# Performance work log

Hardware: AMD Instinct MI355X
Metric: run time of the kernel (lower is better)

The kernel has to match this reference:

```python
import jax, jax.numpy as jnp
import numpy as np

RATIO = 0.2
MIX_ALPHA = 0.5
TEMPERATURE = 0.1
EPS = 1e-12  # F.normalize eps


def setup_inputs() -> dict:
    key = jax.random.key(0)
    z = jax.random.normal(key, (16384, 256), dtype=jnp.float32)
    return {"z": z}


def reference(z):
    B = z.shape[0]
    n_hard = max(1, int(B * RATIO))

    # L2-normalize rows (F.normalize with eps clamp)
    norm = jnp.maximum(jnp.linalg.norm(z, axis=-1, keepdims=True), EPS)
    z_norm = z / norm

    # [B, B] cosine similarity, diagonal excluded
    sim = z_norm @ z_norm.T
    diag = jnp.eye(B, dtype=bool)
    sim = jnp.where(diag, -jnp.inf, sim)
    logits = sim / TEMPERATURE  # softmax(logits) == sim_probs

    # Batched sampling: replaces the per-sample Python loop with one fused pass
    key = jax.random.key(42)
    k_src, k_tgt, k_alpha = jax.random.split(key, 3)
    src_idx = jax.random.randint(k_src, (n_hard,), 0, B)  # torch.randint
    # categorical over logits rows == multinomial over softmax probs
    tgt_idx = jax.random.categorical(k_tgt, logits[src_idx], axis=-1)
    alpha = jax.random.uniform(k_alpha, (n_hard, 1), dtype=z.dtype) * MIX_ALPHA

    hard_negs = alpha * z[src_idx] + (1.0 - alpha) * z[tgt_idx]  # [n_hard, D]
    return hard_negs
```

## Files before the change

kernel.cpp:

```cpp
#include <hip/hip_runtime.h>
#include <stdint.h>
#include <math.h>

#define BN 16384
#define DK 256
#define NH 3276
#define NJB 52
#define NCB 128
#define NTILE (NJB * NCB)

typedef __attribute__((ext_vector_type(8))) short short8;
typedef __attribute__((ext_vector_type(4))) short short4v;
typedef __attribute__((ext_vector_type(4))) float f32x4;

__host__ __device__ __forceinline__ void tf2x32(uint32_t k0, uint32_t k1,
                                                uint32_t c0, uint32_t c1,
                                                uint32_t& o0, uint32_t& o1) {
  uint32_t ks2 = 0x1BD11BDAu ^ k0 ^ k1;
  uint32_t x0 = c0 + k0, x1 = c1 + k1;
#define RR(d) { x0 += x1; x1 = (x1 << d) | (x1 >> (32 - d)); x1 ^= x0; }
  RR(13) RR(15) RR(26) RR(6)   x0 += k1;  x1 += ks2 + 1u;
  RR(17) RR(29) RR(16) RR(24)  x0 += ks2; x1 += k0  + 2u;
  RR(13) RR(15) RR(26) RR(6)   x0 += k0;  x1 += k1  + 3u;
  RR(17) RR(29) RR(16) RR(24)  x0 += k1;  x1 += ks2 + 4u;
  RR(13) RR(15) RR(26) RR(6)   x0 += ks2; x1 += k0  + 5u;
#undef RR
  o0 = x0; o1 = x1;
}

__device__ __forceinline__ uint32_t rand32_at(uint32_t k0, uint32_t k1, uint32_t p) {
  uint32_t x0, x1; tf2x32(k0, k1, 0u, p, x0, x1);
  return x0 ^ x1;
}

__device__ __forceinline__ float unif01_from_bits(uint32_t bits) {
  return __uint_as_float((bits >> 9) | 0x3f800000u) - 1.0f;
}

__device__ __forceinline__ float gumbel_at(uint32_t k0, uint32_t k1, uint32_t p) {
  uint32_t bits = rand32_at(k0, k1, p);
  float f = unif01_from_bits(bits);
  float u = fmaxf(f, 1.17549435e-38f);
  float t = __log2f(u) * (-0.69314718055994531f);
  return __log2f(t) * (-0.69314718055994531f);
}

__device__ __forceinline__ unsigned long long packvc(float v, uint32_t c) {
  uint32_t u = __float_as_uint(v);
  u ^= ((int32_t)u < 0) ? 0xFFFFFFFFu : 0x80000000u;
  return ((unsigned long long)u << 32) | (unsigned long long)(~c);
}

__device__ __forceinline__ void glds16(const unsigned short* g, short* l) {
  __builtin_amdgcn_global_load_lds(
      (const __attribute__((address_space(1))) void*)g,
      (__attribute__((address_space(3))) void*)l, 16, 0, 0);
}

__global__ __launch_bounds__(256) void k_prep(const float* __restrict__ z,
                                              unsigned short* __restrict__ zh,
                                              unsigned short* __restrict__ zl,
                                              int* __restrict__ src_idx,
                                              unsigned long long* __restrict__ best,
                                              uint32_t k20, uint32_t k21) {
  int b = blockIdx.x, t = threadIdx.x;
  if (b < BN / 4) {
    int row = b * 4 + (t >> 6), lane = t & 63;
    float4 v = *(const float4*)&z[row * DK + lane * 4];
    float ss = v.x * v.x + v.y * v.y + v.z * v.z + v.w * v.w;
#pragma unroll
    for (int off = 32; off; off >>= 1) ss += __shfl_xor(ss, off, 64);
    float inv = 1.0f / fmaxf(sqrtf(ss), 1e-12f);
    float f[4] = {v.x * inv, v.y * inv, v.z * inv, v.w * inv};
    short4v h, l;
#pragma unroll
    for (int i = 0; i < 4; ++i) {
      uint32_t u = __float_as_uint(f[i]);
      h[i] = (short)(u >> 16);
      float r = f[i] - __uint_as_float(u & 0xFFFF0000u);
      l[i] = (short)(__float_as_uint(r) >> 16);
    }
    *(short4v*)&zh[row * DK + lane * 4] = h;
    *(short4v*)&zl[row * DK + lane * 4] = l;
  } else {
    int i = (b - BN / 4) * 256 + t;
    if (i < NH) {
      uint32_t bits = rand32_at(k20, k21, (uint32_t)i);
      src_idx[i] = (int)(bits & (uint32_t)(BN - 1));
      best[i] = 0ull;
    }
  }
}

__global__ __launch_bounds__(256, 4) void k_main(const unsigned short* __restrict__ zh,
                                                 const unsigned short* __restrict__ zl,
                                                 const int* __restrict__ src_idx,
                                                 unsigned long long* __restrict__ best,
                                                 uint32_t kt0, uint32_t kt1) {
  __shared__ __align__(16) short As_hi[64 * 32];
  __shared__ __align__(16) short As_lo[64 * 32];
  __shared__ __align__(16) short Bs_hi[128 * 32];
  __shared__ __align__(16) short Bs_lo[128 * 32];

  const int flat = blockIdx.x;
  const int xcd = flat & 7, slot = flat >> 3;
  const int c_base = (xcd * 16 + (slot & 15)) * 128;
  const int j_base = (slot >> 4) * 64;

  const int t = threadIdx.x;
  const int lane = t & 63, w = t >> 6;

  const int ra = w * 16 + (lane >> 2);
  const int rb0 = w * 32 + (lane >> 2);
  const int rb1 = rb0 + 16;
  const int ua = (lane & 3) ^ ((ra >> 1) & 3);
  const int ub0 = (lane & 3) ^ ((rb0 >> 1) & 3);
  const int ub1 = (lane & 3) ^ ((rb1 >> 1) & 3);
  const uint32_t offA = (uint32_t)(src_idx[min(j_base + ra, NH - 1)] * DK + ua * 8);
  const uint32_t offB0 = (uint32_t)((c_base + rb0) * DK + ub0 * 8);
  const uint32_t offB1 = (uint32_t)((c_base + rb1) * DK + ub1 * 8);
  short* dA  = &As_hi[w * 512];
  short* dAl = &As_lo[w * 512];
  short* dB  = &Bs_hi[w * 1024];
  short* dBl = &Bs_lo[w * 1024];

  const int mh = w >> 1, ch = w & 1;
  const int cl = lane & 15, q = lane >> 4;
  int foffA[2], foffB[4];
#pragma unroll
  for (int i = 0; i < 2; ++i) {
    int r = mh * 32 + cl + i * 16;
    foffA[i] = r * 32 + (q ^ ((r >> 1) & 3)) * 8;
  }
#pragma unroll
  for (int i = 0; i < 4; ++i) {
    int r = ch * 64 + cl + i * 16;
    foffB[i] = r * 32 + (q ^ ((r >> 1) & 3)) * 8;
  }

  const int q4 = q * 4;
  const int coff = c_base + ch * 64;
  const int roff = j_base + mh * 32;
  const uint32_t ccl = (uint32_t)(coff + cl);

  f32x4 acc[2][4];
#pragma unroll
  for (int mt = 0; mt < 2; ++mt)
#pragma unroll
    for (int nt = 0; nt < 4; ++nt) acc[mt][nt] = (f32x4){0.f, 0.f, 0.f, 0.f};

  float gum[32];

  glds16(zh + offA, dA);
  glds16(zl + offA, dAl);
  glds16(zh + offB0, dB);
  glds16(zh + offB1, dB + 512);
  glds16(zl + offB0, dBl);
  glds16(zl + offB1, dBl + 512);

#pragma unroll
  for (int kc = 0; kc < 8; ++kc) {
    __syncthreads();

    short8 ah[2], al[2], bh[4], bl[4];
#pragma unroll
    for (int nt = 0; nt < 4; ++nt) {
      bh[nt] = *(const short8*)&Bs_hi[foffB[nt]];
      bl[nt] = *(const short8*)&Bs_lo[foffB[nt]];
    }
#pragma unroll
    for (int mt = 0; mt < 2; ++mt) {
      ah[mt] = *(const short8*)&As_hi[foffA[mt]];
      al[mt] = *(const short8*)&As_lo[foffA[mt]];
    }
    __syncthreads();

    if (kc < 7) {
      const int ko = (kc + 1) * 32;
      glds16(zh + offA + ko, dA);
      glds16(zl + offA + ko, dAl);
      glds16(zh + offB0 + ko, dB);
      glds16(zh + offB1 + ko, dB + 512);
      glds16(zl + offB0 + ko, dBl);
      glds16(zl + offB1 + ko, dBl + 512);
    }

#pragma unroll
    for (int mt = 0; mt < 2; ++mt)
#pragma unroll
      for (int nt = 0; nt < 4; ++nt) {
        acc[mt][nt] = __builtin_amdgcn_mfma_f32_16x16x32_bf16(ah[mt], bh[nt], acc[mt][nt], 0, 0, 0);
        acc[mt][nt] = __builtin_amdgcn_mfma_f32_16x16x32_bf16(ah[mt], bl[nt], acc[mt][nt], 0, 0, 0);
        acc[mt][nt] = __builtin_amdgcn_mfma_f32_16x16x32_bf16(al[mt], bh[nt], acc[mt][nt], 0, 0, 0);
      }

#pragma unroll
    for (int i = 0; i < 4; ++i) {
      const int idx = kc * 4 + i;
      const int mt = idx >> 4, r = (idx >> 2) & 3, nt = idx & 3;
      int gj = roff + mt * 16 + q4 + r;
      uint32_t p = (uint32_t)gj * (uint32_t)BN + ccl + (uint32_t)(nt * 16);
      float gv = gumbel_at(kt0, kt1, p);
      asm volatile("" : "+v"(gv));
      gum[idx] = gv;
    }
  }

#pragma unroll
  for (int mt = 0; mt < 2; ++mt)
#pragma unroll
    for (int r = 0; r < 4; ++r) {
      int gj = roff + mt * 16 + q4 + r;
      int s = src_idx[min(gj, NH - 1)];
      float bv = -INFINITY; uint32_t bc = 0;
#pragma unroll
      for (int nt = 0; nt < 4; ++nt) {
        uint32_t c = ccl + (uint32_t)(nt * 16);
        float tot = fmaf(acc[mt][nt][r], 10.0f, gum[((mt * 4 + r) * 4) + nt]);
        tot = ((int)c == s) ? -INFINITY : tot;
        if (tot > bv) { bv = tot; bc = c; }
      }
      unsigned long long key = packvc(bv, bc);
#pragma unroll
      for (int off = 1; off <= 8; off <<= 1) {
        unsigned long long o = __shfl_xor(key, off, 64);
        if (o > key) key = o;
      }
      if (cl == 0 && gj < NH) atomicMax(&best[gj], key);
    }
}

__global__ __launch_bounds__(64) void k_out(const float* __restrict__ z,
                                            const int* __restrict__ src_idx,
                                            const unsigned long long* __restrict__ best,
                                            float* __restrict__ out,
                                            uint32_t ka0, uint32_t ka1) {
  int j = blockIdx.x;
  int lane = threadIdx.x;
  int s = src_idx[j];
  int tgt = (int)(~((uint32_t)(best[j] & 0xFFFFFFFFull)));
  uint32_t bits = rand32_at(ka0, ka1, (uint32_t)j);
  float alpha = unif01_from_bits(bits) * 0.5f;
  float om = 1.0f - alpha;
  float4 a = *(const float4*)&z[s * DK + lane * 4];
  float4 b = *(const float4*)&z[tgt * DK + lane * 4];
  float4 o;
  o.x = alpha * a.x + om * b.x;
  o.y = alpha * a.y + om * b.y;
  o.z = alpha * a.z + om * b.z;
  o.w = alpha * a.w + om * b.w;
  *(float4*)&out[j * DK + lane * 4] = o;
}

extern "C" void kernel_launch(void* const* d_in, const int* in_sizes, int n_in,
                              void* d_out, int out_size, void* d_ws, size_t ws_size,
                              hipStream_t stream) {
  const float* z = (const float*)d_in[0];
  float* out = (float*)d_out;
  char* ws = (char*)d_ws;
  int*                src_idx = (int*)(ws);
  unsigned long long* best    = (unsigned long long*)(ws + 16384);
  unsigned short*     zh      = (unsigned short*)(ws + 65536);
  unsigned short*     zl      = (unsigned short*)(ws + 65536 + 8388608);

  uint32_t r0 = 0u, r1 = 42u;
  uint32_t ks0, ks1, kt0, kt1, ka0, ka1, k20, k21;
  tf2x32(r0, r1, 0u, 0u, ks0, ks1);
  tf2x32(r0, r1, 0u, 1u, kt0, kt1);
  tf2x32(r0, r1, 0u, 2u, ka0, ka1);
  tf2x32(ks0, ks1, 0u, 1u, k20, k21);

  k_prep<<<dim3(BN / 4 + (NH + 255) / 256), dim3(256), 0, stream>>>(
      z, zh, zl, src_idx, best, k20, k21);
  k_main<<<dim3(NTILE), dim3(256), 0, stream>>>(zh, zl, src_idx, best, kt0, kt1);
  k_out <<<dim3(NH), dim3(64), 0, stream>>>(z, src_idx, best, out, ka0, ka1);
}
```

Measured before the change: 244.6 us.

## Load MFMA operands directly from global memory instead of staging in LDS

```diff
diff --git a/kernel.cpp b/kernel.cpp
--- a/kernel.cpp
+++ b/kernel.cpp
@@ -51,12 +51,6 @@
   return ((unsigned long long)u << 32) | (unsigned long long)(~c);
 }
 
-__device__ __forceinline__ void glds16(const unsigned short* g, short* l) {
-  __builtin_amdgcn_global_load_lds(
-      (const __attribute__((address_space(1))) void*)g,
-      (__attribute__((address_space(3))) void*)l, 16, 0, 0);
-}
-
 __global__ __launch_bounds__(256) void k_prep(const float* __restrict__ z,
                                               unsigned short* __restrict__ zh,
                                               unsigned short* __restrict__ zl,
@@ -97,11 +91,6 @@
                                                  const int* __restrict__ src_idx,
                                                  unsigned long long* __restrict__ best,
                                                  uint32_t kt0, uint32_t kt1) {
-  __shared__ __align__(16) short As_hi[64 * 32];
-  __shared__ __align__(16) short As_lo[64 * 32];
-  __shared__ __align__(16) short Bs_hi[128 * 32];
-  __shared__ __align__(16) short Bs_lo[128 * 32];
-
   const int flat = blockIdx.x;
   const int xcd = flat & 7, slot = flat >> 3;
   const int c_base = (xcd * 16 + (slot & 15)) * 128;
@@ -110,32 +99,20 @@
   const int t = threadIdx.x;
   const int lane = t & 63, w = t >> 6;
 
-  const int ra = w * 16 + (lane >> 2);
-  const int rb0 = w * 32 + (lane >> 2);
-  const int rb1 = rb0 + 16;
-  const int ua = (lane & 3) ^ ((ra >> 1) & 3);
-  const int ub0 = (lane & 3) ^ ((rb0 >> 1) & 3);
-  const int ub1 = (lane & 3) ^ ((rb1 >> 1) & 3);
-  const uint32_t offA = (uint32_t)(src_idx[min(j_base + ra, NH - 1)] * DK + ua * 8);
-  const uint32_t offB0 = (uint32_t)((c_base + rb0) * DK + ub0 * 8);
-  const uint32_t offB1 = (uint32_t)((c_base + rb1) * DK + ub1 * 8);
-  short* dA  = &As_hi[w * 512];
-  short* dAl = &As_lo[w * 512];
-  short* dB  = &Bs_hi[w * 1024];
-  short* dBl = &Bs_lo[w * 1024];
-
   const int mh = w >> 1, ch = w & 1;
   const int cl = lane & 15, q = lane >> 4;
-  int foffA[2], foffB[4];
-#pragma unroll
-  for (int i = 0; i < 2; ++i) {
-    int r = mh * 32 + cl + i * 16;
-    foffA[i] = r * 32 + (q ^ ((r >> 1) & 3)) * 8;
-  }
-#pragma unroll
-  for (int i = 0; i < 4; ++i) {
-    int r = ch * 64 + cl + i * 16;
-    foffB[i] = r * 32 + (q ^ ((r >> 1) & 3)) * 8;
+
+  uint32_t offA[2], offB[4];
+#pragma unroll
+  for (int mt = 0; mt < 2; ++mt) {
+    int r = j_base + mh * 32 + cl + mt * 16;
+    int s = src_idx[min(r, NH - 1)];
+    offA[mt] = (uint32_t)(s * DK + q * 8);
+  }
+#pragma unroll
+  for (int nt = 0; nt < 4; ++nt) {
+    int r = c_base + ch * 64 + cl + nt * 16;
+    offB[nt] = (uint32_t)(r * DK + q * 8);
   }
 
   const int q4 = q * 4;
@@ -151,48 +128,21 @@
 
   float gum[32];
 
-  glds16(zh + offA, dA);
-  glds16(zl + offA, dAl);
-  glds16(zh + offB0, dB);
-  glds16(zh + offB1, dB + 512);
-  glds16(zl + offB0, dBl);
-  glds16(zl + offB1, dBl + 512);
-
 #pragma unroll
   for (int kc = 0; kc < 8; ++kc) {
-    __syncthreads();
+    const int ko = kc * 32;
 
     short8 ah[2], al[2], bh[4], bl[4];
 #pragma unroll
     for (int nt = 0; nt < 4; ++nt) {
-      bh[nt] = *(const short8*)&Bs_hi[foffB[nt]];
-      bl[nt] = *(const short8*)&Bs_lo[foffB[nt]];
+      bh[nt] = *(const short8*)&zh[offB[nt] + ko];
+      bl[nt] = *(const short8*)&zl[offB[nt] + ko];
     }
 #pragma unroll
     for (int mt = 0; mt < 2; ++mt) {
-      ah[mt] = *(const short8*)&As_hi[foffA[mt]];
-      al[mt] = *(const short8*)&As_lo[foffA[mt]];
-    }
-    __syncthreads();
-
-    if (kc < 7) {
-      const int ko = (kc + 1) * 32;
-      glds16(zh + offA + ko, dA);
-      glds16(zl + offA + ko, dAl);
-      glds16(zh + offB0 + ko, dB);
-      glds16(zh + offB1 + ko, dB + 512);
-      glds16(zl + offB0 + ko, dBl);
-      glds16(zl + offB1 + ko, dBl + 512);
-    }
-
-#pragma unroll
-    for (int mt = 0; mt < 2; ++mt)
-#pragma unroll
-      for (int nt = 0; nt < 4; ++nt) {
-        acc[mt][nt] = __builtin_amdgcn_mfma_f32_16x16x32_bf16(ah[mt], bh[nt], acc[mt][nt], 0, 0, 0);
-        acc[mt][nt] = __builtin_amdgcn_mfma_f32_16x16x32_bf16(ah[mt], bl[nt], acc[mt][nt], 0, 0, 0);
-        acc[mt][nt] = __builtin_amdgcn_mfma_f32_16x16x32_bf16(al[mt], bh[nt], acc[mt][nt], 0, 0, 0);
-      }
+      ah[mt] = *(const short8*)&zh[offA[mt] + ko];
+      al[mt] = *(const short8*)&zl[offA[mt] + ko];
+    }
 
 #pragma unroll
     for (int i = 0; i < 4; ++i) {
@@ -204,6 +154,15 @@
       asm volatile("" : "+v"(gv));
       gum[idx] = gv;
     }
+
+#pragma unroll
+    for (int mt = 0; mt < 2; ++mt)
+#pragma unroll
+      for (int nt = 0; nt < 4; ++nt) {
+        acc[mt][nt] = __builtin_amdgcn_mfma_f32_16x16x32_bf16(ah[mt], bh[nt], acc[mt][nt], 0, 0, 0);
+        acc[mt][nt] = __builtin_amdgcn_mfma_f32_16x16x32_bf16(ah[mt], bl[nt], acc[mt][nt], 0, 0, 0);
+        acc[mt][nt] = __builtin_amdgcn_mfma_f32_16x16x32_bf16(al[mt], bh[nt], acc[mt][nt], 0, 0, 0);
+      }
   }
 
 #pragma unroll
```

Measured after the change: 388.7 us. 1.59x slower.
